# Optimization experiments

Measured on AMD Instinct MI355X. Metric: run time of the kernel, lower is better.

## Reference

```python
import jax, jax.numpy as jnp
import numpy as np

N_NODES = 20000
N_EDGES = 640000
IN_DIM = 256
HID = 128
N_GRAPHS = 64


def setup_inputs() -> dict:
    key = jax.random.key(0)
    ks = jax.random.split(key, 9)
    x = jax.random.normal(ks[0], (N_NODES, IN_DIM), jnp.float32)
    edge_index = jax.random.randint(ks[1], (2, N_EDGES), 0, N_NODES, dtype=jnp.int32)
    batch = jnp.sort(jax.random.randint(ks[2], (N_NODES,), 0, N_GRAPHS, dtype=jnp.int32))

    def lin(k, fan_in, fan_out):
        # torch.nn.Linear default init: U(-1/sqrt(fan_in), 1/sqrt(fan_in))
        bound = 1.0 / np.sqrt(fan_in)
        kw, kb = jax.random.split(k)
        W = jax.random.uniform(kw, (fan_in, fan_out), jnp.float32, -bound, bound)
        b = jax.random.uniform(kb, (fan_out,), jnp.float32, -bound, bound)
        return W, b

    W0, b0 = lin(ks[3], IN_DIM, HID)
    W1, b1 = lin(ks[4], HID, HID)
    W2, b2 = lin(ks[5], HID, HID)
    return dict(x=x, edge_index=edge_index, batch=batch,
                W0=W0, b0=b0, W1=W1, b1=b1, W2=W2, b2=b2)


def reference(x, edge_index, batch, W0, b0, W1, b1, W2, b2):
    src, dst = edge_index[0], edge_index[1]
    edge_batch = batch[src]  # [E] segment id per edge
    ones = jnp.ones((edge_batch.shape[0], 1), x.dtype)
    counts = jax.ops.segment_sum(ones, edge_batch, num_segments=N_GRAPHS)
    inv_counts = 1.0 / jnp.maximum(counts, 1.0)

    def pool(z):
        # gather endpoint features, concat -> [E, 2*HID], mean pool by graph
        edge_emb = jnp.concatenate([z[src], z[dst]], axis=1)
        return jax.ops.segment_sum(edge_emb, edge_batch, num_segments=N_GRAPHS) * inv_counts

    g = []
    z = x
    for W, b in ((W0, b0), (W1, b1), (W2, b2)):
        z = z @ W + b
        g.append(pool(z))
    return jnp.concatenate(g, axis=1)  # [N_GRAPHS, 3 * 2 * HID]
```

## Files before the change

### kernel.cpp

```cpp
#include <hip/hip_runtime.h>

#define N_NODES 20000
#define N_EDGES 640000
#define N_GRAPHS 64

#define NCHUNK 128
#define CHUNK_SZ 157
#define GSPLIT 8
#define GSUB 8

#define BG_TILE 2048
#define NBG 313
#define SEGCAP 80
#define GR_CAP 768
#define NSLOT4 (NBG * SEGCAP / 4)

#define CD_OFF      0
#define DEG_OFF     1280000
#define CNT_OFF     1300000
#define Y_OFF       1300064
#define PART_OFF    1316448
#define BH_OFF      3413600
#define VALS_OFF    3433632

__global__ __launch_bounds__(256) void bucket_g_k(const int* __restrict__ ei,
                                                  const int* __restrict__ batch,
                                                  unsigned* __restrict__ vals,
                                                  unsigned* __restrict__ bh,
                                                  float* __restrict__ Y) {
    __shared__ unsigned hist[N_GRAPHS];
    __shared__ unsigned base[N_GRAPHS + 1];
    __shared__ unsigned lv[BG_TILE];
    __shared__ unsigned char gidx[BG_TILE];
    const int t = threadIdx.x;
    const int blk = blockIdx.x;
    if (t < N_GRAPHS) hist[t] = 0u;
    __syncthreads();

    const int e0 = blk * BG_TILE;
    const int ecnt = (e0 + BG_TILE <= N_EDGES) ? BG_TILE : (N_EDGES - e0);
    unsigned pv[8], rnk[8], gg[8];
#pragma unroll
    for (int k = 0; k < 8; ++k) {
        int i = t + k * 256;
        if (i < ecnt) {
            unsigned s = (unsigned)ei[e0 + i];
            unsigned d = (unsigned)ei[N_EDGES + e0 + i];
            unsigned g = (unsigned)batch[s];
            pv[k] = (s << 15) | d;
            gg[k] = g;
            rnk[k] = atomicAdd(&hist[g], 1u);
        } else {
            gg[k] = 0xFFFFFFFFu;
        }
    }
    __syncthreads();
    if (t == 0) {
        unsigned acc = 0u;
        base[0] = 0u;
        for (int g = 0; g < N_GRAPHS; ++g) { acc += hist[g]; base[g + 1] = acc; }
    }
    if (t < N_GRAPHS) {
        unsigned c = hist[t];
        bh[blk * N_GRAPHS + t] = (c > SEGCAP) ? SEGCAP : c;
    }
    __syncthreads();
    if (t < N_GRAPHS) {
        unsigned b0 = base[t], b1 = base[t + 1];
        for (unsigned i = b0; i < b1; ++i) gidx[i] = (unsigned char)t;
    }
#pragma unroll
    for (int k = 0; k < 8; ++k) {
        if (gg[k] != 0xFFFFFFFFu) lv[base[gg[k]] + rnk[k]] = pv[k];
    }
    __syncthreads();
    for (int i = t; i < ecnt; i += 256) {
        unsigned g = gidx[i];
        unsigned slot = (unsigned)i - base[g];
        if (slot < SEGCAP)
            vals[((size_t)g * NBG + blk) * SEGCAP + slot] = lv[i];
    }
    if (blk == 0) {
        float4* y4 = (float4*)Y;
        for (int i = t; i < 64 * 64; i += 256) y4[i] = make_float4(0.f, 0.f, 0.f, 0.f);
    }
}

__global__ __launch_bounds__(1024) void cd_col_k(const unsigned* __restrict__ vals,
                                                 const unsigned* __restrict__ bh,
                                                 const int* __restrict__ batch,
                                                 float* __restrict__ Cdcol,
                                                 float* __restrict__ deg,
                                                 float* __restrict__ counts) {
    __shared__ unsigned scnt[NBG];
    __shared__ unsigned dh[2500];
    __shared__ unsigned sdeg[GR_CAP];
    __shared__ int s_lo, s_hi;
    const int t = threadIdx.x;
    const int g = blockIdx.x >> 2;
    const int q = blockIdx.x & 3;
    const int d0 = q * 5000;

    for (int i = t; i < 2500; i += 1024) dh[i] = 0u;
    if (t < NBG) scnt[t] = bh[t * N_GRAPHS + g];
    if (q == 0) {
        if (t < GR_CAP) sdeg[t] = 0u;
        if (t == 0) {
            int lo = 0, hi = N_NODES;
            while (lo < hi) { int m = (lo + hi) >> 1; if (batch[m] < g) lo = m + 1; else hi = m; }
            s_lo = lo;
            int lo2 = lo; hi = N_NODES;
            while (lo2 < hi) { int m = (lo2 + hi) >> 1; if (batch[m] < g + 1) lo2 = m + 1; else hi = m; }
            s_hi = lo2;
        }
    }
    __syncthreads();
    const int lo = (q == 0) ? s_lo : 0;

    const uint4* v4 = (const uint4*)(vals + (size_t)g * NBG * SEGCAP);
    for (int i = t; i < NSLOT4; i += 1024) {
        uint4 v = *(v4 + i);
        unsigned w = (unsigned)i * 4u;
        unsigned seg = (unsigned)(((unsigned long long)w * 53687092ull) >> 32);
        unsigned local = w - seg * 80u;
        unsigned c = scnt[seg];
#define CD_ONE(VX, L)                                                            \
        if ((L) < c) {                                                           \
            int rd_ = (int)((VX) & 0x7FFFu) - d0;                                \
            if ((unsigned)rd_ < 5000u)                                           \
                atomicAdd(&dh[rd_ >> 1], 1u << ((rd_ & 1) * 16));                \
            if (q == 0) {                                                        \
                int rs_ = (int)((VX) >> 15) - lo;                                \
                if ((unsigned)rs_ < (unsigned)GR_CAP) atomicAdd(&sdeg[rs_], 1u); \
            }                                                                    \
        }
        CD_ONE(v.x, local + 0u)
        CD_ONE(v.y, local + 1u)
        CD_ONE(v.z, local + 2u)
        CD_ONE(v.w, local + 3u)
#undef CD_ONE
    }
    __syncthreads();

    float2* outc = (float2*)(Cdcol + (size_t)g * N_NODES + d0);
    for (int w = t; w < 2500; w += 1024) {
        unsigned v = dh[w];
        outc[w] = make_float2((float)(v & 0xFFFFu), (float)(v >> 16));
    }
    if (q == 0) {
        const int range = s_hi - lo;
        for (int i = t; i < range; i += 1024) deg[lo + i] = (float)sdeg[i];
        if (t == 0) {
            unsigned tot = 0;
            for (int i = 0; i < NBG; ++i) tot += scnt[i];
            counts[g] = (float)tot;
        }
    }
}

#define FMA8(C0, C1, XV)                                          \
    acc[0].x = fmaf(C0.x, XV.x, acc[0].x); acc[0].y = fmaf(C0.x, XV.y, acc[0].y); \
    acc[0].z = fmaf(C0.x, XV.z, acc[0].z); acc[0].w = fmaf(C0.x, XV.w, acc[0].w); \
    acc[1].x = fmaf(C0.y, XV.x, acc[1].x); acc[1].y = fmaf(C0.y, XV.y, acc[1].y); \
    acc[1].z = fmaf(C0.y, XV.z, acc[1].z); acc[1].w = fmaf(C0.y, XV.w, acc[1].w); \
    acc[2].x = fmaf(C0.z, XV.x, acc[2].x); acc[2].y = fmaf(C0.z, XV.y, acc[2].y); \
    acc[2].z = fmaf(C0.z, XV.z, acc[2].z); acc[2].w = fmaf(C0.z, XV.w, acc[2].w); \
    acc[3].x = fmaf(C0.w, XV.x, acc[3].x); acc[3].y = fmaf(C0.w, XV.y, acc[3].y); \
    acc[3].z = fmaf(C0.w, XV.z, acc[3].z); acc[3].w = fmaf(C0.w, XV.w, acc[3].w); \
    acc[4].x = fmaf(C1.x, XV.x, acc[4].x); acc[4].y = fmaf(C1.x, XV.y, acc[4].y); \
    acc[4].z = fmaf(C1.x, XV.z, acc[4].z); acc[4].w = fmaf(C1.x, XV.w, acc[4].w); \
    acc[5].x = fmaf(C1.y, XV.x, acc[5].x); acc[5].y = fmaf(C1.y, XV.y, acc[5].y); \
    acc[5].z = fmaf(C1.y, XV.z, acc[5].z); acc[5].w = fmaf(C1.y, XV.w, acc[5].w); \
    acc[6].x = fmaf(C1.z, XV.x, acc[6].x); acc[6].y = fmaf(C1.z, XV.y, acc[6].y); \
    acc[6].z = fmaf(C1.z, XV.z, acc[6].z); acc[6].w = fmaf(C1.z, XV.w, acc[6].w); \
    acc[7].x = fmaf(C1.w, XV.x, acc[7].x); acc[7].y = fmaf(C1.w, XV.y, acc[7].y); \
    acc[7].z = fmaf(C1.w, XV.z, acc[7].z); acc[7].w = fmaf(C1.w, XV.w, acc[7].w);

__global__ __launch_bounds__(256) void pool_k(const float* __restrict__ x,
                                              const int* __restrict__ batch,
                                              const float* __restrict__ Cdcol,
                                              const float* __restrict__ deg,
                                              float* __restrict__ Y,
                                              float* __restrict__ part) {
    __shared__ float4 sc4[CHUNK_SZ * 2];
    __shared__ float sdeg[CHUNK_SZ];
    __shared__ int   sbatch[CHUNK_SZ];
    __shared__ float4 red[2 * GSUB * 64];

    const int t = threadIdx.x;
    const int fg = t & 63;
    const int p  = t >> 6;
    const int b = blockIdx.x & 127;
    const int j = blockIdx.x >> 7;
    const int n0 = b * CHUNK_SZ;
    const int cnt = (n0 + CHUNK_SZ <= N_NODES) ? CHUNK_SZ : (N_NODES - n0);

    float* sc = (float*)sc4;
    const float* cbase = Cdcol + (size_t)(j * GSUB) * N_NODES + n0;
#pragma unroll
    for (int k = 0; k < GSUB; ++k)
        for (int i = t; i < cnt; i += 256)
            sc[i * GSUB + k] = cbase[(size_t)k * N_NODES + i];
    if (j == 0) {
        for (int i = t; i < cnt; i += 256) {
            sdeg[i] = deg[n0 + i];
            sbatch[i] = batch[n0 + i];
        }
    }
    __syncthreads();

    const float4* xp = (const float4*)x + (size_t)n0 * 64 + fg;
#define XL(I) xp[(size_t)(I) * 64]
    float4 acc[GSUB];
#pragma unroll
    for (int k = 0; k < GSUB; ++k) acc[k] = make_float4(0.f, 0.f, 0.f, 0.f);

    if (j == 0) {
        float4 accs = make_float4(0.f, 0.f, 0.f, 0.f);
        int gprev = (p < cnt) ? sbatch[p] : 0;
        int i = p;
        float4 xn = make_float4(0.f, 0.f, 0.f, 0.f);
        if (i < cnt) xn = XL(i);
        for (; i < cnt; i += 4) {
            float4 xv = xn;
            if (i + 4 < cnt) xn = XL(i + 4);
            int g = sbatch[i];
            if (g != gprev) {
                float* yr = Y + gprev * 256 + fg * 4;
                atomicAdd(yr + 0, accs.x); atomicAdd(yr + 1, accs.y);
                atomicAdd(yr + 2, accs.z); atomicAdd(yr + 3, accs.w);
                accs = make_float4(0.f, 0.f, 0.f, 0.f);
                gprev = g;
            }
            float dg = sdeg[i];
            accs.x = fmaf(dg, xv.x, accs.x); accs.y = fmaf(dg, xv.y, accs.y);
            accs.z = fmaf(dg, xv.z, accs.z); accs.w = fmaf(dg, xv.w, accs.w);
            float4 c0 = sc4[i * 2], c1 = sc4[i * 2 + 1];
            FMA8(c0, c1, xv)
        }
        if (p < cnt) {
            float* yr = Y + gprev * 256 + fg * 4;
            atomicAdd(yr + 0, accs.x); atomicAdd(yr + 1, accs.y);
            atomicAdd(yr + 2, accs.z); atomicAdd(yr + 3, accs.w);
        }
    } else {
        int i = p;
        float4 xa, xb, xc, xd;
        if (i      < cnt) xa = XL(i);
        if (i + 4  < cnt) xb = XL(i + 4);
        if (i + 8  < cnt) xc = XL(i + 8);
        if (i + 12 < cnt) xd = XL(i + 12);
        for (; i + 12 < cnt; i += 16) {
            float4 y0 = xa, y1 = xb, y2 = xc, y3 = xd;
            if (i + 16 < cnt) xa = XL(i + 16);
            if (i + 20 < cnt) xb = XL(i + 20);
            if (i + 24 < cnt) xc = XL(i + 24);
            if (i + 28 < cnt) xd = XL(i + 28);
            {
                float4 c0 = sc4[i * 2], c1 = sc4[i * 2 + 1];
                FMA8(c0, c1, y0)
            }
            {
                float4 c0 = sc4[(i + 4) * 2], c1 = sc4[(i + 4) * 2 + 1];
                FMA8(c0, c1, y1)
            }
            {
                float4 c0 = sc4[(i + 8) * 2], c1 = sc4[(i + 8) * 2 + 1];
                FMA8(c0, c1, y2)
            }
            {
                float4 c0 = sc4[(i + 12) * 2], c1 = sc4[(i + 12) * 2 + 1];
                FMA8(c0, c1, y3)
            }
        }
        for (; i < cnt; i += 4) {
            float4 xv = XL(i);
            float4 c0 = sc4[i * 2], c1 = sc4[i * 2 + 1];
            FMA8(c0, c1, xv)
        }
    }
#undef XL

    if (p >= 2) {
#pragma unroll
        for (int k = 0; k < GSUB; ++k) red[(p - 2) * (GSUB * 64) + k * 64 + fg] = acc[k];
    }
    __syncthreads();
    if (p < 2) {
#pragma unroll
        for (int k = 0; k < GSUB; ++k) {
            float4 v = red[p * (GSUB * 64) + k * 64 + fg];
            acc[k].x += v.x; acc[k].y += v.y; acc[k].z += v.z; acc[k].w += v.w;
        }
    }
    __syncthreads();
    if (p == 1) {
#pragma unroll
        for (int k = 0; k < GSUB; ++k) red[k * 64 + fg] = acc[k];
    }
    __syncthreads();
    if (p == 0) {
        float4* part4 = (float4*)part;
#pragma unroll
        for (int k = 0; k < GSUB; ++k) {
            float4 v = red[k * 64 + fg];
            acc[k].x += v.x; acc[k].y += v.y; acc[k].z += v.z; acc[k].w += v.w;
            part4[(size_t)(b * 64 + j * GSUB + k) * 64 + fg] = acc[k];
        }
    }
}

__global__ __launch_bounds__(256) void chain2_k(const float* __restrict__ Y,
                                                const float* __restrict__ part,
                                                const float* __restrict__ counts,
                                                const float* __restrict__ W0, const float* __restrict__ b0,
                                                const float* __restrict__ W1, const float* __restrict__ b1,
                                                const float* __restrict__ W2, const float* __restrict__ b2,
                                                float* __restrict__ out) {
    __shared__ float m[256];
    __shared__ float h[128];
    const int r = blockIdx.x;
    const int t = threadIdx.x;
    const int g = r & 63;
    const int half = (r >= 64) ? 128 : 0;

    float c = counts[g];
    float inv = 1.0f / fmaxf(c, 1.0f);
    float beta = c * inv;

    if (r < 64) {
        m[t] = Y[r * 256 + t] * inv;
    } else {
        float s = 0.0f;
        for (int bb = 0; bb < NCHUNK; ++bb) s += part[(size_t)(bb * 64 + g) * 256 + t];
        m[t] = s * inv;
    }
    __syncthreads();

    if (t < 128) {
        float s1 = 0.0f;
        for (int k = 0; k < 256; ++k) s1 += m[k] * W0[k * 128 + t];
        s1 += beta * b0[t];
        out[g * 768 + 0 + half + t] = s1;
        h[t] = s1;
    }
    __syncthreads();
    float s2 = 0.0f;
    if (t < 128) {
        for (int k = 0; k < 128; ++k) s2 += h[k] * W1[k * 128 + t];
        s2 += beta * b1[t];
        out[g * 768 + 256 + half + t] = s2;
    }
    __syncthreads();
    if (t < 128) h[t] = s2;
    __syncthreads();
    if (t < 128) {
        float s3 = 0.0f;
        for (int k = 0; k < 128; ++k) s3 += h[k] * W2[k * 128 + t];
        s3 += beta * b2[t];
        out[g * 768 + 512 + half + t] = s3;
    }
}

extern "C" void kernel_launch(void* const* d_in, const int* in_sizes, int n_in,
                              void* d_out, int out_size, void* d_ws, size_t ws_size,
                              hipStream_t stream) {
    const float* x     = (const float*)d_in[0];
    const int*   ei    = (const int*)d_in[1];
    const int*   batch = (const int*)d_in[2];
    const float* W0    = (const float*)d_in[3];
    const float* b0    = (const float*)d_in[4];
    const float* W1    = (const float*)d_in[5];
    const float* b1    = (const float*)d_in[6];
    const float* W2    = (const float*)d_in[7];
    const float* b2    = (const float*)d_in[8];
    float* out = (float*)d_out;

    float*    ws     = (float*)d_ws;
    float*    Cdcol  = ws + CD_OFF;
    float*    deg    = ws + DEG_OFF;
    float*    counts = ws + CNT_OFF;
    float*    Y      = ws + Y_OFF;
    float*    part   = ws + PART_OFF;
    unsigned* bh     = (unsigned*)(ws + BH_OFF);
    unsigned* vals   = (unsigned*)(ws + VALS_OFF);

    bucket_g_k<<<NBG, 256, 0, stream>>>(ei, batch, vals, bh, Y);
    cd_col_k<<<N_GRAPHS * 4, 1024, 0, stream>>>(vals, bh, batch, Cdcol, deg, counts);
    pool_k<<<NCHUNK * GSPLIT, 256, 0, stream>>>(x, batch, Cdcol, deg, Y, part);
    chain2_k<<<128, 256, 0, stream>>>(Y, part, counts, W0, b0, W1, b1, W2, b2, out);
}
```

Baseline: 126.1 us.

## Replace bucket-sort count pipeline with direct global float atomics

Removes the two-kernel bucket sort (per-block graph bucketing plus per-graph column histograms) and instead zeroes the workspace with a memset, then accumulates Cd column counts, node degrees and per-graph edge counts straight into global memory with float atomics. This drops the intermediate vals/bh buffers and one launch, and it also drops the SEGCAP truncation the old code applied to per-block graph buckets. The cost is 1.28M global atomics scattered over a roughly 5 MB matrix, plus a 5 MB memset, in place of shared-memory atomics.

```diff
diff --git a/kernel.cpp b/kernel.cpp
--- a/kernel.cpp
+++ b/kernel.cpp
@@ -8,153 +8,51 @@
 #define CHUNK_SZ 157
 #define GSPLIT 8
 #define GSUB 8
-
-#define BG_TILE 2048
-#define NBG 313
-#define SEGCAP 80
-#define GR_CAP 768
-#define NSLOT4 (NBG * SEGCAP / 4)
 
 #define CD_OFF      0
 #define DEG_OFF     1280000
 #define CNT_OFF     1300000
 #define Y_OFF       1300064
 #define PART_OFF    1316448
-#define BH_OFF      3413600
-#define VALS_OFF    3433632
-
-__global__ __launch_bounds__(256) void bucket_g_k(const int* __restrict__ ei,
-                                                  const int* __restrict__ batch,
-                                                  unsigned* __restrict__ vals,
-                                                  unsigned* __restrict__ bh,
-                                                  float* __restrict__ Y) {
+#define ZERO_F32    1316448
+
+__global__ __launch_bounds__(256) void count_k(const int* __restrict__ ei,
+                                               const int* __restrict__ batch,
+                                               float* __restrict__ Cdcol,
+                                               float* __restrict__ deg,
+                                               float* __restrict__ counts) {
     __shared__ unsigned hist[N_GRAPHS];
-    __shared__ unsigned base[N_GRAPHS + 1];
-    __shared__ unsigned lv[BG_TILE];
-    __shared__ unsigned char gidx[BG_TILE];
     const int t = threadIdx.x;
-    const int blk = blockIdx.x;
     if (t < N_GRAPHS) hist[t] = 0u;
     __syncthreads();
 
-    const int e0 = blk * BG_TILE;
-    const int ecnt = (e0 + BG_TILE <= N_EDGES) ? BG_TILE : (N_EDGES - e0);
-    unsigned pv[8], rnk[8], gg[8];
-#pragma unroll
-    for (int k = 0; k < 8; ++k) {
-        int i = t + k * 256;
-        if (i < ecnt) {
-            unsigned s = (unsigned)ei[e0 + i];
-            unsigned d = (unsigned)ei[N_EDGES + e0 + i];
-            unsigned g = (unsigned)batch[s];
-            pv[k] = (s << 15) | d;
-            gg[k] = g;
-            rnk[k] = atomicAdd(&hist[g], 1u);
-        } else {
-            gg[k] = 0xFFFFFFFFu;
-        }
-    }
-    __syncthreads();
-    if (t == 0) {
-        unsigned acc = 0u;
-        base[0] = 0u;
-        for (int g = 0; g < N_GRAPHS; ++g) { acc += hist[g]; base[g + 1] = acc; }
-    }
+    const int e0 = blockIdx.x * 1024 + t * 4;
+    const int4 s4 = *(const int4*)(ei + e0);
+    const int4 d4 = *(const int4*)(ei + N_EDGES + e0);
+
+    const int g0 = batch[s4.x];
+    const int g1 = batch[s4.y];
+    const int g2 = batch[s4.z];
+    const int g3 = batch[s4.w];
+
+    atomicAdd(&Cdcol[(size_t)g0 * N_NODES + d4.x], 1.0f);
+    atomicAdd(&Cdcol[(size_t)g1 * N_NODES + d4.y], 1.0f);
+    atomicAdd(&Cdcol[(size_t)g2 * N_NODES + d4.z], 1.0f);
+    atomicAdd(&Cdcol[(size_t)g3 * N_NODES + d4.w], 1.0f);
+
+    atomicAdd(&deg[s4.x], 1.0f);
+    atomicAdd(&deg[s4.y], 1.0f);
+    atomicAdd(&deg[s4.z], 1.0f);
+    atomicAdd(&deg[s4.w], 1.0f);
+
+    atomicAdd(&hist[g0], 1u);
+    atomicAdd(&hist[g1], 1u);
+    atomicAdd(&hist[g2], 1u);
+    atomicAdd(&hist[g3], 1u);
+    __syncthreads();
     if (t < N_GRAPHS) {
         unsigned c = hist[t];
-        bh[blk * N_GRAPHS + t] = (c > SEGCAP) ? SEGCAP : c;
-    }
-    __syncthreads();
-    if (t < N_GRAPHS) {
-        unsigned b0 = base[t], b1 = base[t + 1];
-        for (unsigned i = b0; i < b1; ++i) gidx[i] = (unsigned char)t;
-    }
-#pragma unroll
-    for (int k = 0; k < 8; ++k) {
-        if (gg[k] != 0xFFFFFFFFu) lv[base[gg[k]] + rnk[k]] = pv[k];
-    }
-    __syncthreads();
-    for (int i = t; i < ecnt; i += 256) {
-        unsigned g = gidx[i];
-        unsigned slot = (unsigned)i - base[g];
-        if (slot < SEGCAP)
-            vals[((size_t)g * NBG + blk) * SEGCAP + slot] = lv[i];
-    }
-    if (blk == 0) {
-        float4* y4 = (float4*)Y;
-        for (int i = t; i < 64 * 64; i += 256) y4[i] = make_float4(0.f, 0.f, 0.f, 0.f);
-    }
-}
-
-__global__ __launch_bounds__(1024) void cd_col_k(const unsigned* __restrict__ vals,
-                                                 const unsigned* __restrict__ bh,
-                                                 const int* __restrict__ batch,
-                                                 float* __restrict__ Cdcol,
-                                                 float* __restrict__ deg,
-                                                 float* __restrict__ counts) {
-    __shared__ unsigned scnt[NBG];
-    __shared__ unsigned dh[2500];
-    __shared__ unsigned sdeg[GR_CAP];
-    __shared__ int s_lo, s_hi;
-    const int t = threadIdx.x;
-    const int g = blockIdx.x >> 2;
-    const int q = blockIdx.x & 3;
-    const int d0 = q * 5000;
-
-    for (int i = t; i < 2500; i += 1024) dh[i] = 0u;
-    if (t < NBG) scnt[t] = bh[t * N_GRAPHS + g];
-    if (q == 0) {
-        if (t < GR_CAP) sdeg[t] = 0u;
-        if (t == 0) {
-            int lo = 0, hi = N_NODES;
-            while (lo < hi) { int m = (lo + hi) >> 1; if (batch[m] < g) lo = m + 1; else hi = m; }
-            s_lo = lo;
-            int lo2 = lo; hi = N_NODES;
-            while (lo2 < hi) { int m = (lo2 + hi) >> 1; if (batch[m] < g + 1) lo2 = m + 1; else hi = m; }
-            s_hi = lo2;
-        }
-    }
-    __syncthreads();
-    const int lo = (q == 0) ? s_lo : 0;
-
-    const uint4* v4 = (const uint4*)(vals + (size_t)g * NBG * SEGCAP);
-    for (int i = t; i < NSLOT4; i += 1024) {
-        uint4 v = *(v4 + i);
-        unsigned w = (unsigned)i * 4u;
-        unsigned seg = (unsigned)(((unsigned long long)w * 53687092ull) >> 32);
-        unsigned local = w - seg * 80u;
-        unsigned c = scnt[seg];
-#define CD_ONE(VX, L)                                                            \
-        if ((L) < c) {                                                           \
-            int rd_ = (int)((VX) & 0x7FFFu) - d0;                                \
-            if ((unsigned)rd_ < 5000u)                                           \
-                atomicAdd(&dh[rd_ >> 1], 1u << ((rd_ & 1) * 16));                \
-            if (q == 0) {                                                        \
-                int rs_ = (int)((VX) >> 15) - lo;                                \
-                if ((unsigned)rs_ < (unsigned)GR_CAP) atomicAdd(&sdeg[rs_], 1u); \
-            }                                                                    \
-        }
-        CD_ONE(v.x, local + 0u)
-        CD_ONE(v.y, local + 1u)
-        CD_ONE(v.z, local + 2u)
-        CD_ONE(v.w, local + 3u)
-#undef CD_ONE
-    }
-    __syncthreads();
-
-    float2* outc = (float2*)(Cdcol + (size_t)g * N_NODES + d0);
-    for (int w = t; w < 2500; w += 1024) {
-        unsigned v = dh[w];
-        outc[w] = make_float2((float)(v & 0xFFFFu), (float)(v >> 16));
-    }
-    if (q == 0) {
-        const int range = s_hi - lo;
-        for (int i = t; i < range; i += 1024) deg[lo + i] = (float)sdeg[i];
-        if (t == 0) {
-            unsigned tot = 0;
-            for (int i = 0; i < NBG; ++i) tot += scnt[i];
-            counts[g] = (float)tot;
-        }
+        if (c) atomicAdd(&counts[t], (float)c);
     }
 }
 
@@ -376,17 +274,15 @@
     const float* b2    = (const float*)d_in[8];
     float* out = (float*)d_out;
 
-    float*    ws     = (float*)d_ws;
-    float*    Cdcol  = ws + CD_OFF;
-    float*    deg    = ws + DEG_OFF;
-    float*    counts = ws + CNT_OFF;
-    float*    Y      = ws + Y_OFF;
-    float*    part   = ws + PART_OFF;
-    unsigned* bh     = (unsigned*)(ws + BH_OFF);
-    unsigned* vals   = (unsigned*)(ws + VALS_OFF);
-
-    bucket_g_k<<<NBG, 256, 0, stream>>>(ei, batch, vals, bh, Y);
-    cd_col_k<<<N_GRAPHS * 4, 1024, 0, stream>>>(vals, bh, batch, Cdcol, deg, counts);
+    float* ws     = (float*)d_ws;
+    float* Cdcol  = ws + CD_OFF;
+    float* deg    = ws + DEG_OFF;
+    float* counts = ws + CNT_OFF;
+    float* Y      = ws + Y_OFF;
+    float* part   = ws + PART_OFF;
+
+    hipMemsetAsync(ws, 0, (size_t)ZERO_F32 * sizeof(float), stream);
+    count_k<<<N_EDGES / 1024, 256, 0, stream>>>(ei, batch, Cdcol, deg, counts);
     pool_k<<<NCHUNK * GSPLIT, 256, 0, stream>>>(x, batch, Cdcol, deg, Y, part);
     chain2_k<<<128, 256, 0, stream>>>(Y, part, counts, W0, b0, W1, b1, W2, b2, out);
 }
```

New measurement: 181.8 us. +44.2%, slower.
